# Performance work log

Measured on AMD Instinct MI355X. Metric: run time of the kernel, lower is better.

Reference implementation:

```python
import jax, jax.numpy as jnp
import numpy as np
from jax import lax

TAU = 2.0      # LIF decay constant (source: tau = 2.0)
V_TH = 1.0     # spikingjelly LIFNode default threshold
ALPHA = 2.0    # ATan surrogate default alpha
BN_EPS = 1e-5


@jax.custom_vjp
def spike(v):
    # Heaviside with ATan surrogate gradient (spikingjelly surrogate.ATan)
    return (v >= V_TH).astype(v.dtype)

def _spike_fwd(v):
    return spike(v), v

def _spike_bwd(v, g):
    x = (jnp.pi / 2.0) * ALPHA * (v - V_TH)
    return (g * (ALPHA / 2.0) / (1.0 + x * x),)

spike.defvjp(_spike_fwd, _spike_bwd)


def lif_step(v, x):
    # leaky integrate: v += (x - (v - v_reset)) / tau, v_reset = 0
    v = v + (x - v) / TAU
    s = spike(v)
    # hard reset to 0; detach_reset=True -> stop_gradient on s in the reset path
    v = v * (1.0 - lax.stop_gradient(s))
    return v, s


def multistep_lif(x_seq):
    # x_seq: (T, ...) ; membrane state carried across T, initial v = 0
    v0 = jnp.zeros_like(x_seq[0])
    _, s_seq = lax.scan(lif_step, v0, x_seq)
    return s_seq


def setup_inputs() -> dict:
    key = jax.random.key(0)
    ks = jax.random.split(key, 3)
    bs, length, c_num, hidden = 64, 128, 32, 256
    x = jax.random.normal(ks[0], (bs, length, c_num), dtype=jnp.float32)
    conv_w = jax.random.normal(ks[1], (hidden, 1, 1, 3), dtype=jnp.float32) * 0.3
    conv_b = jnp.zeros((hidden,), jnp.float32)
    bn_gamma = jnp.ones((hidden,), jnp.float32)
    bn_beta = jnp.zeros((hidden,), jnp.float32)
    bn_mean = jnp.zeros((hidden,), jnp.float32)
    bn_var = jnp.ones((hidden,), jnp.float32)
    lin_w = jax.random.normal(ks[2], (hidden, hidden), dtype=jnp.float32) * (1.0 / np.sqrt(hidden))
    lin_b = jnp.zeros((hidden,), jnp.float32)
    return {"x": x, "conv_w": conv_w, "conv_b": conv_b, "bn_gamma": bn_gamma,
            "bn_beta": bn_beta, "bn_mean": bn_mean, "bn_var": bn_var,
            "lin_w": lin_w, "lin_b": lin_b}


def reference(x, conv_w, conv_b, bn_gamma, bn_beta, bn_mean, bn_var, lin_w, lin_b):
    bs, length, c_num = x.shape
    hidden = conv_w.shape[0]

    # ---- ConvEncoder ----
    xi = jnp.transpose(x, (0, 2, 1))[:, None]  # (bs, 1, c_num, length)
    enc = lax.conv_general_dilated(
        xi, conv_w, window_strides=(1, 1), padding=((0, 0), (1, 1)),
        dimension_numbers=("NCHW", "OIHW", "NCHW"))
    enc = enc + conv_b[None, :, None, None]
    # BatchNorm2d (eval mode, running stats)
    inv = bn_gamma * lax.rsqrt(bn_var + BN_EPS)
    enc = (enc - bn_mean[None, :, None, None]) * inv[None, :, None, None] + bn_beta[None, :, None, None]
    # multi-step LIF over channel dim T = hidden (as in source permute(1,0,2,3))
    enc = jnp.transpose(enc, (1, 0, 2, 3))          # (hidden, bs, c_num, length)
    spks_enc = multistep_lif(enc)                   # (hidden, bs, c_num, length)

    # ---- reshape to per-(bs*c_num) sequences of length `length` with feature hidden ----
    h = jnp.transpose(spks_enc, (1, 2, 3, 0)).reshape(bs * c_num, length, hidden)

    # ---- SpikeRNNCell recurrence over time (Linear + stateful LIF) ----
    def rnn_step(v, x_t):                           # x_t: (N, hidden)
        z = x_t @ lin_w.T + lin_b
        v = v + (z - v) / TAU
        s = spike(v)
        v = v * (1.0 - lax.stop_gradient(s))
        return v, s

    v0 = jnp.zeros((bs * c_num, hidden), x.dtype)
    _, s_seq = lax.scan(rnn_step, v0, jnp.transpose(h, (1, 0, 2)))  # (length, N, hidden)
    spks = s_seq[-1]                                # final-step spikes (N, hidden)

    spks = spks.reshape(bs, c_num * hidden, -1)     # (bs, c_num*hidden, 1)
    return jnp.transpose(spks, (0, 2, 1)), spks[:, :, -1]
```

## Files before the change

kernel.cpp:

```cpp
#include <hip/hip_runtime.h>
#include <stdint.h>

typedef unsigned short u16;
typedef unsigned int u32;
typedef unsigned long long u64;
typedef unsigned char u8;

typedef __attribute__((ext_vector_type(4))) int   i32x4;
typedef __attribute__((ext_vector_type(8))) int   i32x8;
typedef __attribute__((ext_vector_type(4))) float f32x4;

#define OFF_SBITS 0u
#define SBITS_BYTES (2048u * 128u * 32u)
#define OFF_WQ4  (SBITS_BYTES)
#define WQ4_BYTES (2u * 32768u)
#define OFF_SCL  (OFF_WQ4 + WQ4_BYTES)

__global__ __launch_bounds__(256) void prep_enc_kernel(
    const float* __restrict__ x,
    const float* __restrict__ conv_w, const float* __restrict__ conv_b,
    const float* __restrict__ gamma,  const float* __restrict__ beta,
    const float* __restrict__ mean,   const float* __restrict__ var,
    const float* __restrict__ lin_w,  uint8_t* __restrict__ ws,
    u64* __restrict__ sbits) {
    int tid = threadIdx.x;
    int blk = blockIdx.x;
    if (blk < 256) {
        __shared__ float red[256];
        __shared__ u8 nib[256];
        int j = blk, k = tid;
        float wv = lin_w[j * 256 + k];
        red[k] = fabsf(wv);
        __syncthreads();
        #pragma unroll
        for (int s = 128; s > 0; s >>= 1) {
            if (k < s) red[k] = fmaxf(red[k], red[k + s]);
            __syncthreads();
        }
        float m = red[0];
        float S = (m > 0.f) ? 6.0f / m : 0.f;
        float v6 = wv * S;
        float av = fabsf(v6);
        int code;
        if      (av < 0.25f) code = 0;
        else if (av < 0.75f) code = 1;
        else if (av < 1.25f) code = 2;
        else if (av < 1.75f) code = 3;
        else if (av < 2.5f)  code = 4;
        else if (av < 3.5f)  code = 5;
        else if (av < 5.0f)  code = 6;
        else                 code = 7;
        nib[k] = (u8)(((v6 < 0.f && code) ? 8 : 0) | code);
        __syncthreads();
        if (k < 128) {
            u8 byte = (u8)(nib[2 * k] | (nib[2 * k + 1] << 4));
            int ks = k >> 6, kb = (k >> 4) & 3, bi = k & 15;
            (ws + OFF_WQ4)[ks * 32768 + (j * 4 + kb) * 16 + bi] = byte;
        }
        if (k == 0) ((float*)(ws + OFF_SCL))[j] = m * (1.0f / 12.0f);
    } else {
        __shared__ float4 cfl[256];
        {
            int h = tid;
            float inv = gamma[h] / sqrtf(var[h] + 1e-5f);
            float K = (conv_b[h] - mean[h]) * inv + beta[h];
            cfl[h] = make_float4(conv_w[h * 3 + 0] * inv * 0.5f,
                                 conv_w[h * 3 + 1] * inv * 0.5f,
                                 conv_w[h * 3 + 2] * inv * 0.5f, K * 0.5f);
        }
        int p = (blk - 256) * 256 + tid;
        int c = p & 31;
        int l = (p >> 5) & 127;
        int b0 = p >> 12;
        int xb = b0 * 4096 + l * 32 + c;
        float xb0 = x[xb],            xb1 = x[xb + 131072];
        float xa0 = (l > 0)   ? x[xb - 32]          : 0.f;
        float xa1 = (l > 0)   ? x[xb + 131072 - 32] : 0.f;
        float xc0 = (l < 127) ? x[xb + 32]          : 0.f;
        float xc1 = (l < 127) ? x[xb + 131072 + 32] : 0.f;
        u64* d0 = sbits + ((size_t)(b0 * 32 + c) * 128 + (size_t)l) * 4;
        u64* d1 = d0 + (size_t)1024 * 512;

        __syncthreads();
        float v0 = 0.f, v1 = 0.f;
        u64 cur0 = 0ull, cur1 = 0ull;
        #pragma unroll 8
        for (int h = 0; h < 256; ++h) {
            float4 a = cfl[h];
            float e0 = fmaf(a.x, xa0, fmaf(a.y, xb0, fmaf(a.z, xc0, a.w)));
            float e1 = fmaf(a.x, xa1, fmaf(a.y, xb1, fmaf(a.z, xc1, a.w)));
            v0 = fmaf(0.5f, v0, e0);
            v1 = fmaf(0.5f, v1, e1);
            bool s0 = (v0 >= 1.0f);
            bool s1 = (v1 >= 1.0f);
            cur0 |= ((u64)(s0 ? 1u : 0u)) << (h & 63);
            cur1 |= ((u64)(s1 ? 1u : 0u)) << (h & 63);
            if ((h & 63) == 63) {
                d0[h >> 6] = cur0; d1[h >> 6] = cur1;
                cur0 = 0ull; cur1 = 0ull;
            }
            v0 = s0 ? 0.f : v0;
            v1 = s1 ? 0.f : v1;
        }
    }
}

__device__ __forceinline__ u32 spread_nib(u32 byte) {
    u32 x = (byte | (byte << 12)) & 0x000F000Fu;
    x = (x | (x << 6)) & 0x03030303u;
    x = (x | (x << 3)) & 0x11111111u;
    return x << 1;
}

__global__ __launch_bounds__(256, 2) void gemm_scan_kernel(
    const u64* __restrict__ sbits,
    const uint4* __restrict__ wq4,
    const float* __restrict__ lin_b,
    const float* __restrict__ sclp,
    float* __restrict__ out) {
    __shared__ __align__(16) uint8_t smem[36864];
    u32* Awords = (u32*)smem;

    int tid  = threadIdx.x;
    int n    = blockIdx.x;
    int lane = tid & 63;
    int w    = tid >> 6;
    int l15  = lane & 15;
    int quad = lane >> 4;
    int lb   = w * 256 + l15 * 4 + quad;

    float bias = lin_b[tid];
    float sc   = sclp[tid];

    i32x4 bb[2][4];
    #pragma unroll
    for (int ks = 0; ks < 2; ++ks)
        #pragma unroll
        for (int nf = 0; nf < 4; ++nf)
            bb[ks][nf] = ((const i32x4*)wq4)[(size_t)(ks * 2048 + nf * 64 + lb)];

    __builtin_amdgcn_global_load_lds(
        (const __attribute__((address_space(1))) u32*)
            ((const u64*)sbits + (size_t)n * 512 + tid * 2),
        (__attribute__((address_space(3))) u32*)(smem + w * 1024), 16, 0, 0);

    f32x4 acc[8][4];
    #pragma unroll
    for (int mf = 0; mf < 8; ++mf)
        #pragma unroll
        for (int nf = 0; nf < 4; ++nf) {
            f32x4 z = {0.f, 0.f, 0.f, 0.f};
            acc[mf][nf] = z;
        }

    __syncthreads();

    u32 aw[8][2];
    #pragma unroll
    for (int mf = 0; mf < 8; ++mf)
        #pragma unroll
        for (int ks = 0; ks < 2; ++ks)
            aw[mf][ks] = Awords[(mf * 16 + l15) * 8 + ks * 4 + quad];

    #pragma unroll
    for (int ks = 0; ks < 2; ++ks) {
        #pragma unroll
        for (int mf = 0; mf < 8; ++mf) {
            u32 wbits = aw[mf][ks];
            i32x8 afr;
            afr[0] = (int)spread_nib(wbits & 0xFFu);
            afr[1] = (int)spread_nib((wbits >> 8) & 0xFFu);
            afr[2] = (int)spread_nib((wbits >> 16) & 0xFFu);
            afr[3] = (int)spread_nib(wbits >> 24);
            afr[4] = 0; afr[5] = 0; afr[6] = 0; afr[7] = 0;
            #pragma unroll
            for (int nf = 0; nf < 4; ++nf) {
                i32x8 bfr;
                bfr[0] = bb[ks][nf][0]; bfr[1] = bb[ks][nf][1];
                bfr[2] = bb[ks][nf][2]; bfr[3] = bb[ks][nf][3];
                bfr[4] = 0; bfr[5] = 0; bfr[6] = 0; bfr[7] = 0;
                acc[mf][nf] = __builtin_amdgcn_mfma_scale_f32_16x16x128_f8f6f4(
                    afr, bfr, acc[mf][nf], 4, 4,
                    0, 0x7F7F7F7F, 0, 0x7F7F7F7F);
            }
        }
    }

    __syncthreads();

    float* ZW = (float*)(smem + (size_t)w * 9216);
    float zsc = sc;
    float zbi = 0.5f * bias;
    float v = 0.f, sOut = 0.f;
    #pragma unroll
    for (int ph = 0; ph < 4; ++ph) {
        #pragma unroll
        for (int mm = 0; mm < 2; ++mm) {
            int mf = ph * 2 + mm;
            #pragma unroll
            for (int nf = 0; nf < 4; ++nf)
                *(f32x4*)(ZW + (nf * 16 + l15) * 36 + mm * 16 + quad * 4) =
                    acc[mf][nf];
        }
        float zh[32];
        #pragma unroll
        for (int g = 0; g < 8; ++g) {
            f32x4 z4 = *(const f32x4*)(ZW + lane * 36 + g * 4);
            #pragma unroll
            for (int r = 0; r < 4; ++r)
                zh[g * 4 + r] = fmaf(z4[r], zsc, zbi);
        }
        #pragma unroll
        for (int tl = 0; tl < 32; ++tl) {
            v = fmaf(0.5f, v, zh[tl]);
            bool s = (v >= 1.0f);
            if (ph == 3 && tl == 31) sOut = s ? 1.f : 0.f;
            v = s ? 0.f : v;
        }
    }
    out[(size_t)n * 256 + tid]           = sOut;
    out[524288u + (size_t)n * 256 + tid] = sOut;
}

extern "C" void kernel_launch(void* const* d_in, const int* in_sizes, int n_in,
                              void* d_out, int out_size, void* d_ws, size_t ws_size,
                              hipStream_t stream) {
    const float* x      = (const float*)d_in[0];
    const float* conv_w = (const float*)d_in[1];
    const float* conv_b = (const float*)d_in[2];
    const float* gamma  = (const float*)d_in[3];
    const float* beta   = (const float*)d_in[4];
    const float* mean   = (const float*)d_in[5];
    const float* var    = (const float*)d_in[6];
    const float* lin_w  = (const float*)d_in[7];
    const float* lin_b  = (const float*)d_in[8];
    uint8_t* ws = (uint8_t*)d_ws;
    float* out = (float*)d_out;

    hipLaunchKernelGGL(prep_enc_kernel, dim3(768), dim3(256), 0, stream,
                       x, conv_w, conv_b, gamma, beta, mean, var, lin_w,
                       ws, (u64*)(ws + OFF_SBITS));
    hipLaunchKernelGGL(gemm_scan_kernel, dim3(2048), dim3(256), 0, stream,
                       (const u64*)(ws + OFF_SBITS),
                       (const uint4*)(ws + OFF_WQ4), lin_b,
                       (const float*)(ws + OFF_SCL), out);
}
```

Measured before the change: 115.3 us.

## Interleave per-chunk MFMA with LIF scan and shrink accumulators for occupancy

The GEMM now runs one 16-row chunk at a time, both K-halves per chunk, into a double-buffered accumulator. Each chunk's LIF scan overlaps the next chunk's MFMAs, replacing the full 8x4 accumulator array. This cuts accumulator registers and the shared-memory staging buffer, so launch bounds ask for 3 blocks per CU instead of 2. The cost is more LDS round trips per chunk and a scan that still runs serially per thread.

```diff
diff --git a/kernel.cpp b/kernel.cpp
--- a/kernel.cpp
+++ b/kernel.cpp
@@ -112,13 +112,13 @@
     return x << 1;
 }
 
-__global__ __launch_bounds__(256, 2) void gemm_scan_kernel(
+__global__ __launch_bounds__(256, 3) void gemm_scan_kernel(
     const u64* __restrict__ sbits,
     const uint4* __restrict__ wq4,
     const float* __restrict__ lin_b,
     const float* __restrict__ sclp,
     float* __restrict__ out) {
-    __shared__ __align__(16) uint8_t smem[36864];
+    __shared__ __align__(16) uint8_t smem[24576];
     u32* Awords = (u32*)smem;
 
     int tid  = threadIdx.x;
@@ -132,26 +132,17 @@
     float bias = lin_b[tid];
     float sc   = sclp[tid];
 
-    i32x4 bb[2][4];
-    #pragma unroll
-    for (int ks = 0; ks < 2; ++ks)
-        #pragma unroll
-        for (int nf = 0; nf < 4; ++nf)
-            bb[ks][nf] = ((const i32x4*)wq4)[(size_t)(ks * 2048 + nf * 64 + lb)];
-
     __builtin_amdgcn_global_load_lds(
         (const __attribute__((address_space(1))) u32*)
             ((const u64*)sbits + (size_t)n * 512 + tid * 2),
         (__attribute__((address_space(3))) u32*)(smem + w * 1024), 16, 0, 0);
 
-    f32x4 acc[8][4];
+    i32x4 bb[2][4];
     #pragma unroll
-    for (int mf = 0; mf < 8; ++mf)
-        #pragma unroll
-        for (int nf = 0; nf < 4; ++nf) {
-            f32x4 z = {0.f, 0.f, 0.f, 0.f};
-            acc[mf][nf] = z;
-        }
+    for (int ks = 0; ks < 2; ++ks)
+        #pragma unroll
+        for (int nf = 0; nf < 4; ++nf)
+            bb[ks][nf] = ((const i32x4*)wq4)[(size_t)(ks * 2048 + nf * 64 + lb)];
 
     __syncthreads();
 
@@ -162,62 +153,71 @@
         for (int ks = 0; ks < 2; ++ks)
             aw[mf][ks] = Awords[(mf * 16 + l15) * 8 + ks * 4 + quad];
 
-    #pragma unroll
-    for (int ks = 0; ks < 2; ++ks) {
-        #pragma unroll
-        for (int mf = 0; mf < 8; ++mf) {
-            u32 wbits = aw[mf][ks];
-            i32x8 afr;
-            afr[0] = (int)spread_nib(wbits & 0xFFu);
-            afr[1] = (int)spread_nib((wbits >> 8) & 0xFFu);
-            afr[2] = (int)spread_nib((wbits >> 16) & 0xFFu);
-            afr[3] = (int)spread_nib(wbits >> 24);
-            afr[4] = 0; afr[5] = 0; afr[6] = 0; afr[7] = 0;
-            #pragma unroll
-            for (int nf = 0; nf < 4; ++nf) {
-                i32x8 bfr;
-                bfr[0] = bb[ks][nf][0]; bfr[1] = bb[ks][nf][1];
-                bfr[2] = bb[ks][nf][2]; bfr[3] = bb[ks][nf][3];
-                bfr[4] = 0; bfr[5] = 0; bfr[6] = 0; bfr[7] = 0;
-                acc[mf][nf] = __builtin_amdgcn_mfma_scale_f32_16x16x128_f8f6f4(
-                    afr, bfr, acc[mf][nf], 4, 4,
-                    0, 0x7F7F7F7F, 0, 0x7F7F7F7F);
-            }
-        }
-    }
-
-    __syncthreads();
-
-    float* ZW = (float*)(smem + (size_t)w * 9216);
+    float* ZW = (float*)(smem + 4096 + (size_t)w * 5120);
     float zsc = sc;
     float zbi = 0.5f * bias;
+
+#define COMPUTE_CHUNK(MF, ACC)                                               \
+    do {                                                                     \
+        u32 wb0 = aw[MF][0], wb1 = aw[MF][1];                                \
+        i32x8 a0, a1;                                                        \
+        a0[0] = (int)spread_nib(wb0 & 0xFFu);                                \
+        a0[1] = (int)spread_nib((wb0 >> 8) & 0xFFu);                         \
+        a0[2] = (int)spread_nib((wb0 >> 16) & 0xFFu);                        \
+        a0[3] = (int)spread_nib(wb0 >> 24);                                  \
+        a0[4] = 0; a0[5] = 0; a0[6] = 0; a0[7] = 0;                          \
+        a1[0] = (int)spread_nib(wb1 & 0xFFu);                                \
+        a1[1] = (int)spread_nib((wb1 >> 8) & 0xFFu);                         \
+        a1[2] = (int)spread_nib((wb1 >> 16) & 0xFFu);                        \
+        a1[3] = (int)spread_nib(wb1 >> 24);                                  \
+        a1[4] = 0; a1[5] = 0; a1[6] = 0; a1[7] = 0;                          \
+        _Pragma("unroll")                                                    \
+        for (int nf = 0; nf < 4; ++nf) {                                     \
+            i32x8 b0, b1;                                                    \
+            b0[0] = bb[0][nf][0]; b0[1] = bb[0][nf][1];                      \
+            b0[2] = bb[0][nf][2]; b0[3] = bb[0][nf][3];                      \
+            b0[4] = 0; b0[5] = 0; b0[6] = 0; b0[7] = 0;                      \
+            b1[0] = bb[1][nf][0]; b1[1] = bb[1][nf][1];                      \
+            b1[2] = bb[1][nf][2]; b1[3] = bb[1][nf][3];                      \
+            b1[4] = 0; b1[5] = 0; b1[6] = 0; b1[7] = 0;                      \
+            f32x4 t = {0.f, 0.f, 0.f, 0.f};                                  \
+            t = __builtin_amdgcn_mfma_scale_f32_16x16x128_f8f6f4(            \
+                a0, b0, t, 4, 4, 0, 0x7F7F7F7F, 0, 0x7F7F7F7F);              \
+            t = __builtin_amdgcn_mfma_scale_f32_16x16x128_f8f6f4(            \
+                a1, b1, t, 4, 4, 0, 0x7F7F7F7F, 0, 0x7F7F7F7F);              \
+            ACC[nf] = t;                                                     \
+        }                                                                    \
+    } while (0)
+
+    f32x4 acc[2][4];
+    COMPUTE_CHUNK(0, acc[0]);
+
     float v = 0.f, sOut = 0.f;
     #pragma unroll
-    for (int ph = 0; ph < 4; ++ph) {
-        #pragma unroll
-        for (int mm = 0; mm < 2; ++mm) {
-            int mf = ph * 2 + mm;
-            #pragma unroll
-            for (int nf = 0; nf < 4; ++nf)
-                *(f32x4*)(ZW + (nf * 16 + l15) * 36 + mm * 16 + quad * 4) =
-                    acc[mf][nf];
-        }
-        float zh[32];
-        #pragma unroll
-        for (int g = 0; g < 8; ++g) {
-            f32x4 z4 = *(const f32x4*)(ZW + lane * 36 + g * 4);
+    for (int mf = 0; mf < 8; ++mf) {
+        int cur = mf & 1, nxt = cur ^ 1;
+        if (mf < 7) COMPUTE_CHUNK(mf + 1, acc[nxt]);
+        #pragma unroll
+        for (int nf = 0; nf < 4; ++nf)
+            *(f32x4*)(ZW + (nf * 16 + l15) * 20 + quad * 4) = acc[cur][nf];
+        float zh[16];
+        #pragma unroll
+        for (int g = 0; g < 4; ++g) {
+            f32x4 z4 = *(const f32x4*)(ZW + lane * 20 + g * 4);
             #pragma unroll
             for (int r = 0; r < 4; ++r)
                 zh[g * 4 + r] = fmaf(z4[r], zsc, zbi);
         }
         #pragma unroll
-        for (int tl = 0; tl < 32; ++tl) {
+        for (int tl = 0; tl < 16; ++tl) {
             v = fmaf(0.5f, v, zh[tl]);
             bool s = (v >= 1.0f);
-            if (ph == 3 && tl == 31) sOut = s ? 1.f : 0.f;
+            if (mf == 7 && tl == 15) sOut = s ? 1.f : 0.f;
             v = s ? 0.f : v;
         }
     }
+#undef COMPUTE_CHUNK
+
     out[(size_t)n * 256 + tid]           = sOut;
     out[524288u + (size_t)n * 256 + tid] = sOut;
 }
```

After: 116.1 us. No clear change (+0.8%).
